# Kernel optimization log

Measured on AMD Instinct MI355X. Metric: run time of the kernel, lower is better.

## Reference

```python
import jax, jax.numpy as jnp
import numpy as np

K_SIZE = 5  # local patch size


def extract_patches(x, k):
    """im2col-style k x k patch extraction with SAME zero padding.
    x: [B,H,W,C] -> [B,H,W,k*k,C]"""
    B, H, W, C = x.shape
    pad = k // 2
    xp = jnp.pad(x, ((0, 0), (pad, pad), (pad, pad), (0, 0)))
    # loop over fixed k*k offsets (25), stacked along a new patch axis
    slices = [xp[:, i:i + H, j:j + W, :] for i in range(k) for j in range(k)]
    return jnp.stack(slices, axis=3)  # [B,H,W,k*k,C]


def setup_inputs() -> dict:
    key = jax.random.key(0)
    k1, k2, k3 = jax.random.split(key, 3)
    B, H, W, C, BIN = 2, 128, 128, 64, 64
    return {
        "main": jax.random.normal(k1, (B, H, W, C), dtype=jnp.float32),
        "ref": jax.random.normal(k2, (B, H, W, C), dtype=jnp.float32),
        "ref_value": jax.random.normal(k3, (B, H, W, BIN), dtype=jnp.float32),
    }


def reference(main, ref, ref_value):
    k = K_SIZE
    ref_stacked = extract_patches(ref, k)            # [B,H,W,k*k,C]
    ref_value_stacked = extract_patches(ref_value, k)  # [B,H,W,k*k,BIN]
    # dot-product attention over the k*k patch axis
    scores = jnp.einsum('bhwpc,bhwc->bhwp', ref_stacked, main)  # [B,H,W,k*k]
    attn = jax.nn.softmax(scores, axis=3)
    # attention-weighted sum of value patches
    out = jnp.einsum('bhwp,bhwpv->bhwv', attn, ref_value_stacked)  # [B,H,W,BIN]
    return out
```

## Files before the change

kernel.cpp:

```cpp
#include <hip/hip_runtime.h>


#define BB 2
#define HH 128
#define WW 128
#define CC 64
#define KK 5
#define PAD 2
#define TC 20
#define NV (KK * TC)

template <int CTRL>
__device__ __forceinline__ float dpp_add(float v) {
    int r = __builtin_amdgcn_update_dpp(0, __float_as_int(v), CTRL, 0xF, 0xF, true);
    return v + __int_as_float(r);
}

__device__ __forceinline__ float group16_sum(float v) {
    v = dpp_add<0xB1>(v);
    v = dpp_add<0x4E>(v);
    v = dpp_add<0x124>(v);
    v = dpp_add<0x128>(v);
    return v;
}

__device__ __forceinline__ void stage_tile(const float* __restrict__ src,
                                           float* __restrict__ lds,
                                           int b, int h, int w0,
                                           int grp, int lane16) {
    #pragma unroll
    for (int i = 0; i < 7; ++i) {
        const int v = grp + 16 * i;
        if (v < NV) {
            const int r   = v / TC;
            const int c   = v - r * TC;
            const int hg  = h + r - PAD;
            const int wg  = w0 + c - PAD;
            const int hgc = min(max(hg, 0), HH - 1);
            const int wgc = min(max(wg, 0), WW - 1);
            const float4 d = *reinterpret_cast<const float4*>(
                src + (((size_t)(b * HH + hgc)) * WW + wgc) * CC + lane16 * 4);
            const bool ok = ((unsigned)hg < (unsigned)HH) &
                            ((unsigned)wg < (unsigned)WW);
            float4 z;
            z.x = ok ? d.x : 0.0f;
            z.y = ok ? d.y : 0.0f;
            z.z = ok ? d.z : 0.0f;
            z.w = ok ? d.w : 0.0f;
            *reinterpret_cast<float4*>(lds + (size_t)v * CC + lane16 * 4) = z;
        }
    }
}

__global__ __launch_bounds__(256, 4) void local_attn_kernel(
    const float* __restrict__ mainp,
    const float* __restrict__ refp,
    const float* __restrict__ refvp,
    float* __restrict__ outp)
{
    __shared__ float tile[NV * CC];

    const int tid    = threadIdx.x;
    const int lane16 = tid & 15;
    const int pix    = tid >> 4;
    const int seg    = blockIdx.x;
    const int wseg   = seg & 7;
    const int h      = (seg >> 3) & (HH - 1);
    const int b      = seg >> 10;
    const int w0     = wseg * 16;
    const int w      = w0 + pix;
    const int cb     = lane16 * 4;

    const size_t pbase = (((size_t)(b * HH + h)) * WW + w) * CC + cb;
    const float4 m4 = *reinterpret_cast<const float4*>(mainp + pbase);

    stage_tile(refp, tile, b, h, w0, pix, lane16);
    __syncthreads();

    const float* tbase = tile + (size_t)pix * CC + cb;

    float sc[KK * KK];
    #pragma unroll
    for (int r = 0; r < KK; ++r) {
        #pragma unroll
        for (int dj = 0; dj < KK; ++dj) {
            const float4 t =
                *reinterpret_cast<const float4*>(tbase + (r * TC + dj) * CC);
            sc[r * KK + dj] = m4.x * t.x + m4.y * t.y + m4.z * t.z + m4.w * t.w;
        }
    }

    #pragma unroll
    for (int p = 0; p < KK * KK; ++p) sc[p] = group16_sum(sc[p]);

    float mx = sc[0];
    #pragma unroll
    for (int p = 1; p < KK * KK; ++p) mx = fmaxf(mx, sc[p]);
    float s = 0.0f;
    #pragma unroll
    for (int p = 0; p < KK * KK; ++p) { sc[p] = __expf(sc[p] - mx); s += sc[p]; }
    const float inv = 1.0f / s;
    #pragma unroll
    for (int p = 0; p < KK * KK; ++p) sc[p] *= inv;

    __syncthreads();
    stage_tile(refvp, tile, b, h, w0, pix, lane16);
    __syncthreads();

    float4 acc = make_float4(0.f, 0.f, 0.f, 0.f);
    #pragma unroll
    for (int r = 0; r < KK; ++r) {
        #pragma unroll
        for (int dj = 0; dj < KK; ++dj) {
            const float4 t =
                *reinterpret_cast<const float4*>(tbase + (r * TC + dj) * CC);
            const float a = sc[r * KK + dj];
            acc.x += a * t.x;
            acc.y += a * t.y;
            acc.z += a * t.z;
            acc.w += a * t.w;
        }
    }

    *reinterpret_cast<float4*>(outp + pbase) = acc;
}

extern "C" void kernel_launch(void* const* d_in, const int* in_sizes, int n_in,
                              void* d_out, int out_size, void* d_ws, size_t ws_size,
                              hipStream_t stream) {
    const float* mainp = (const float*)d_in[0];
    const float* refp  = (const float*)d_in[1];
    const float* refvp = (const float*)d_in[2];
    float* outp        = (float*)d_out;

    const int blocks = BB * HH * (WW / 16);
    local_attn_kernel<<<blocks, 256, 0, stream>>>(mainp, refp, refvp, outp);
}
```

Before: 82.89 us.

## Read value patches directly from global memory and fast-path interior tiles

Stops staging the ref_value tile in LDS. Each thread now gathers its 25 value vectors straight from global memory and relies on the cache for reuse, which removes two block barriers and an LDS write pass. An interior fast path skips clamping and masking when loading both ref and value, and softmax normalisation is applied once to the output accumulator instead of to every weight. The cost is 25 uncoalesced-per-pixel global loads per thread and separate boundary and interior code paths, which may add divergence in edge blocks.

```diff
diff --git a/kernel.cpp b/kernel.cpp
--- a/kernel.cpp
+++ b/kernel.cpp
@@ -24,41 +24,13 @@
     return v;
 }
 
-__device__ __forceinline__ void stage_tile(const float* __restrict__ src,
-                                           float* __restrict__ lds,
-                                           int b, int h, int w0,
-                                           int grp, int lane16) {
-    #pragma unroll
-    for (int i = 0; i < 7; ++i) {
-        const int v = grp + 16 * i;
-        if (v < NV) {
-            const int r   = v / TC;
-            const int c   = v - r * TC;
-            const int hg  = h + r - PAD;
-            const int wg  = w0 + c - PAD;
-            const int hgc = min(max(hg, 0), HH - 1);
-            const int wgc = min(max(wg, 0), WW - 1);
-            const float4 d = *reinterpret_cast<const float4*>(
-                src + (((size_t)(b * HH + hgc)) * WW + wgc) * CC + lane16 * 4);
-            const bool ok = ((unsigned)hg < (unsigned)HH) &
-                            ((unsigned)wg < (unsigned)WW);
-            float4 z;
-            z.x = ok ? d.x : 0.0f;
-            z.y = ok ? d.y : 0.0f;
-            z.z = ok ? d.z : 0.0f;
-            z.w = ok ? d.w : 0.0f;
-            *reinterpret_cast<float4*>(lds + (size_t)v * CC + lane16 * 4) = z;
-        }
-    }
-}
-
 __global__ __launch_bounds__(256, 4) void local_attn_kernel(
     const float* __restrict__ mainp,
     const float* __restrict__ refp,
     const float* __restrict__ refvp,
     float* __restrict__ outp)
 {
-    __shared__ float tile[NV * CC];
+    __shared__ float reft[NV * CC];
 
     const int tid    = threadIdx.x;
     const int lane16 = tid & 15;
@@ -74,11 +46,50 @@
     const size_t pbase = (((size_t)(b * HH + h)) * WW + w) * CC + cb;
     const float4 m4 = *reinterpret_cast<const float4*>(mainp + pbase);
 
-    stage_tile(refp, tile, b, h, w0, pix, lane16);
+    const bool interior = (wseg >= 1) & (wseg <= 6) & (h >= PAD) & (h < HH - PAD);
+
+    {
+        int r = 0, c = pix;
+        if (interior) {
+            const float* srcb =
+                refp + (((size_t)(b * HH + h - PAD)) * WW + (w0 - PAD)) * CC + cb;
+            #pragma unroll
+            for (int i = 0; i < 7; ++i) {
+                const int v = pix + 16 * i;
+                if (v < NV) {
+                    const float4 d = *reinterpret_cast<const float4*>(
+                        srcb + ((size_t)(r * WW + c)) * CC);
+                    *reinterpret_cast<float4*>(reft + (size_t)v * CC + cb) = d;
+                }
+                c += 16; const bool wr = (c >= TC); c = wr ? c - TC : c; r += wr;
+            }
+        } else {
+            #pragma unroll
+            for (int i = 0; i < 7; ++i) {
+                const int v = pix + 16 * i;
+                if (v < NV) {
+                    const int hg  = h + r - PAD;
+                    const int wg  = w0 + c - PAD;
+                    const int hgc = min(max(hg, 0), HH - 1);
+                    const int wgc = min(max(wg, 0), WW - 1);
+                    const float4 d = *reinterpret_cast<const float4*>(
+                        refp + (((size_t)(b * HH + hgc)) * WW + wgc) * CC + cb);
+                    const bool ok = ((unsigned)hg < (unsigned)HH) &
+                                    ((unsigned)wg < (unsigned)WW);
+                    float4 z;
+                    z.x = ok ? d.x : 0.0f;
+                    z.y = ok ? d.y : 0.0f;
+                    z.z = ok ? d.z : 0.0f;
+                    z.w = ok ? d.w : 0.0f;
+                    *reinterpret_cast<float4*>(reft + (size_t)v * CC + cb) = z;
+                }
+                c += 16; const bool wr = (c >= TC); c = wr ? c - TC : c; r += wr;
+            }
+        }
+    }
     __syncthreads();
 
-    const float* tbase = tile + (size_t)pix * CC + cb;
-
+    const float* tbase = reft + pix * CC + cb;
     float sc[KK * KK];
     #pragma unroll
     for (int r = 0; r < KK; ++r) {
@@ -96,31 +107,56 @@
     float mx = sc[0];
     #pragma unroll
     for (int p = 1; p < KK * KK; ++p) mx = fmaxf(mx, sc[p]);
-    float s = 0.0f;
+    float ssum = 0.0f;
     #pragma unroll
-    for (int p = 0; p < KK * KK; ++p) { sc[p] = __expf(sc[p] - mx); s += sc[p]; }
-    const float inv = 1.0f / s;
-    #pragma unroll
-    for (int p = 0; p < KK * KK; ++p) sc[p] *= inv;
-
-    __syncthreads();
-    stage_tile(refvp, tile, b, h, w0, pix, lane16);
-    __syncthreads();
+    for (int p = 0; p < KK * KK; ++p) { sc[p] = __expf(sc[p] - mx); ssum += sc[p]; }
+    const float inv = 1.0f / ssum;
 
     float4 acc = make_float4(0.f, 0.f, 0.f, 0.f);
-    #pragma unroll
-    for (int r = 0; r < KK; ++r) {
+    if (interior) {
+        const float* vb = refvp + pbase;
+        #pragma unroll
+        for (int di = 0; di < KK; ++di) {
+            const float* row = vb + (ptrdiff_t)(di - PAD) * (WW * CC);
+            #pragma unroll
+            for (int dj = 0; dj < KK; ++dj) {
+                const float4 v4 =
+                    *reinterpret_cast<const float4*>(row + (dj - PAD) * CC);
+                const float a = sc[di * KK + dj];
+                acc.x += a * v4.x;
+                acc.y += a * v4.y;
+                acc.z += a * v4.z;
+                acc.w += a * v4.w;
+            }
+        }
+    } else {
+        int   wwc[KK];
+        float wokf[KK];
         #pragma unroll
         for (int dj = 0; dj < KK; ++dj) {
-            const float4 t =
-                *reinterpret_cast<const float4*>(tbase + (r * TC + dj) * CC);
-            const float a = sc[r * KK + dj];
-            acc.x += a * t.x;
-            acc.y += a * t.y;
-            acc.z += a * t.z;
-            acc.w += a * t.w;
+            const int ww_ = w + dj - PAD;
+            wwc[dj]  = min(max(ww_, 0), WW - 1);
+            wokf[dj] = ((unsigned)ww_ < (unsigned)WW) ? 1.0f : 0.0f;
+        }
+        #pragma unroll
+        for (int di = 0; di < KK; ++di) {
+            const int hh_  = h + di - PAD;
+            const int hhc  = min(max(hh_, 0), HH - 1);
+            const float hokf = ((unsigned)hh_ < (unsigned)HH) ? 1.0f : 0.0f;
+            const float* row = refvp + (((size_t)(b * HH + hhc)) * WW) * CC + cb;
+            #pragma unroll
+            for (int dj = 0; dj < KK; ++dj) {
+                const float4 v4 =
+                    *reinterpret_cast<const float4*>(row + (size_t)wwc[dj] * CC);
+                const float a = sc[di * KK + dj] * hokf * wokf[dj];
+                acc.x += a * v4.x;
+                acc.y += a * v4.y;
+                acc.z += a * v4.z;
+                acc.w += a * v4.w;
+            }
         }
     }
+    acc.x *= inv; acc.y *= inv; acc.z *= inv; acc.w *= inv;
 
     *reinterpret_cast<float4*>(outp + pbase) = acc;
 }
```

New measurement: 82.68 us. About the same (-0.3%).
